# Performance work log

Hardware: AMD Instinct MI355X
Metric: run time of the kernel (lower is better)

The kernel has to match this reference:

```python
import jax, jax.numpy as jnp
import numpy as np

D = 768      # d_model
S = 8192     # wordpiece positions
N = 8192     # character rows
T = 1024     # words (token ids 1..T)
F = 16       # max_form_len
L = 8        # max_tag_len
XV = 50257   # xtokenizer vocab
CV = 512     # char vocab
TV = 512     # tag vocab


def setup_inputs() -> dict:
    key = jax.random.key(0)
    ks = jax.random.split(key, 16)
    xtokens = jax.random.randint(ks[0], (1, S), 0, XV)
    # tokens[:,:,0]=word id 1..T (each word owns a contiguous run of chars),
    # tokens[:,:,1]=xtoken position in [0,S), tokens[:,:,2]=char id
    tok_ids = (jnp.arange(N) * T) // N + 1
    xtok_ids = jax.random.randint(ks[1], (N,), 0, S)
    char_ids = jax.random.randint(ks[2], (N,), 0, CV)
    tokens = jnp.stack([tok_ids, xtok_ids, char_ids], axis=-1)[None]
    target_form_chars = jax.random.randint(ks[3], (1, T * F), 0, CV)
    target_tags = jax.random.randint(ks[4], (1, T * L), 0, TV)
    special_symbols = jnp.arange(4, dtype=jnp.int32)
    sc = 1.0 / np.sqrt(D)
    return {
        "xtokens": xtokens,
        "tokens": tokens,
        "special_symbols": special_symbols,
        "max_form_len": F,
        "max_tag_len": L,
        "target_form_chars": target_form_chars,
        "target_tags": target_tags,
        "xemb": jax.random.normal(ks[5], (XV, D), jnp.float32) * sc,
        "W_enc": jax.random.normal(ks[6], (D, D), jnp.float32) * sc,
        "b_enc": jnp.zeros((D,), jnp.float32),
        "char_emb": jax.random.normal(ks[7], (CV, D), jnp.float32) * sc,
        "tag_emb": jax.random.normal(ks[8], (TV, D), jnp.float32) * sc,
        "W_s": jax.random.normal(ks[9], (D, D), jnp.float32) * sc,
        "W_c": jax.random.normal(ks[10], (D, D), jnp.float32) * sc,
        "form_pos": jax.random.normal(ks[11], (F, D), jnp.float32) * sc,
        "tag_pos": jax.random.normal(ks[12], (L, D), jnp.float32) * sc,
        "W_char": jax.random.normal(ks[13], (D, CV), jnp.float32) * sc,
        "W_tag": jax.random.normal(ks[14], (D, TV), jnp.float32) * sc,
    }


def reference(xtokens, tokens, special_symbols, max_form_len, max_tag_len,
              target_form_chars, target_tags,
              xemb, W_enc, b_enc, char_emb, tag_emb,
              W_s, W_c, form_pos, tag_pos, W_char, W_tag):
    n_tok = target_form_chars.shape[1] // max_form_len  # = T (static)
    # xmodel: contextual encoding of wordpieces -> token_ctx [1,S,D]
    token_ctx = jnp.tanh(xemb[xtokens] @ W_enc + b_enc)
    # Vectorized replacement of the while-loop: per-word segment mean over
    # the xtoken positions of that word's characters (boolean-mask gather).
    seg = tokens[0, :, 0] - 1                     # [N] word index 0..T-1
    gathered = token_ctx[0][tokens[0, :, 1]]      # [N,D] gather ctx per char
    ones = jnp.ones((gathered.shape[0],), gathered.dtype)
    cnt = jax.ops.segment_sum(ones, seg, num_segments=n_tok)        # [T]
    token_state = jax.ops.segment_sum(gathered, seg, num_segments=n_tok)
    token_state = token_state / cnt[:, None]      # [T,D] mean-pooled state
    # character-level summary of input_chars (col 2), same segment mean
    char_in = char_emb[tokens[0, :, 2]]           # [N,D]
    char_state = jax.ops.segment_sum(char_in, seg, num_segments=n_tok)
    char_state = char_state / cnt[:, None]
    state = jnp.tanh(token_state @ W_s + char_state @ W_c)          # [T,D]
    # tagger decoding with teacher forcing on the sliced target sequences
    tgt_c = char_emb[target_form_chars[0].reshape(n_tok, max_form_len)]
    h_c = jnp.tanh(state[:, None, :] + form_pos[None, :, :] + tgt_c)
    seg_scores = (h_c @ W_char).reshape(1, n_tok * max_form_len, W_char.shape[1])
    tgt_t = tag_emb[target_tags[0].reshape(n_tok, max_tag_len)]
    h_t = jnp.tanh(state[:, None, :] + tag_pos[None, :, :] + tgt_t)
    tag_scores = (h_t @ W_tag).reshape(1, n_tok * max_tag_len, W_tag.shape[1])
    return seg_scores, tag_scores
```

## Files before the change

### kernel.cpp

```cpp
#include <hip/hip_runtime.h>
#include <hip/hip_bf16.h>

#define DD 768
#define NN 8192
#define TT 1024
#define FF 16
#define LL 8
#define CVV 512
#define TVV 512

typedef __attribute__((ext_vector_type(8))) short bf16x8;
typedef __attribute__((ext_vector_type(4))) float f32x4;

__device__ inline unsigned short f2bf(float f) {
    union { float f; unsigned u; } v; v.f = f;
    unsigned r = v.u + 0x7fffu + ((v.u >> 16) & 1u);
    return (unsigned short)(r >> 16);
}

__device__ inline float fast_tanh(float x) {
    float e2 = __expf(2.0f * x);
    return (e2 - 1.0f) * __builtin_amdgcn_rcpf(e2 + 1.0f);
}

__device__ inline void async16(const void* g, void* l) {
    __builtin_amdgcn_global_load_lds(
        (const __attribute__((address_space(1))) unsigned int*)g,
        (__attribute__((address_space(3))) unsigned int*)l, 16, 0, 0);
}

#define GEMM_PROLOG(COLT)                                                    \
    __shared__ short As[128 * 32];                                           \
    __shared__ short Bs[128 * 32];                                           \
    const int bcol = (blockIdx.x % (COLT)) * 128;                            \
    const int brow = (blockIdx.x / (COLT)) * 128;                            \
    const int t = threadIdx.x, lane = t & 63, wid = t >> 6;                  \
    const int wr = (wid >> 1) * 64, wc = (wid & 1) * 64;                     \
    const int l15 = lane & 15, lk8 = (lane >> 4) * 8;                        \
    const int strow = t >> 2, skb = (t & 3) * 8;                             \
    short* al0 = &As[t * 8];                                                 \
    short* al1 = &As[2048 + t * 8];                                          \
    short* bl0 = &Bs[t * 8];                                                 \
    short* bl1 = &Bs[2048 + t * 8];                                          \
    f32x4 acc[4][4] = {};

#define MFMA_TILE_CORE()                                                     \
    {                                                                        \
        bf16x8 afr[4], bfr[4];                                               \
        _Pragma("unroll")                                                    \
        for (int m = 0; m < 4; ++m)                                          \
            afr[m] = *(const bf16x8*)&As[(wr + m * 16 + l15) * 32 + lk8];    \
        _Pragma("unroll")                                                    \
        for (int n = 0; n < 4; ++n)                                          \
            bfr[n] = *(const bf16x8*)&Bs[(wc + n * 16 + l15) * 32 + lk8];    \
        _Pragma("unroll")                                                    \
        for (int m = 0; m < 4; ++m)                                          \
            _Pragma("unroll")                                                \
            for (int n = 0; n < 4; ++n)                                      \
                acc[m][n] = __builtin_amdgcn_mfma_f32_16x16x32_bf16(         \
                    afr[m], bfr[n], acc[m][n], 0, 0, 0);                     \
    }

#define GEMM_KLOOP(KTOT, APTR, BPTR, K)                                      \
    {                                                                        \
        const short* ag0 = (APTR) + (size_t)(brow + strow) * (K) + skb;      \
        const short* ag1 = (APTR) + (size_t)(brow + strow + 64) * (K) + skb; \
        const short* bg0 = (BPTR) + (size_t)(bcol + strow) * (K) + skb;      \
        const short* bg1 = (BPTR) + (size_t)(bcol + strow + 64) * (K) + skb; \
        for (int k0 = 0; k0 < (KTOT); k0 += 32) {                            \
            __syncthreads();                                                 \
            async16(ag0 + k0, al0);                                          \
            async16(ag1 + k0, al1);                                          \
            async16(bg0 + k0, bl0);                                          \
            async16(bg1 + k0, bl1);                                          \
            __syncthreads();                                                 \
            MFMA_TILE_CORE();                                                \
        }                                                                    \
    }

template<int M, int N, int K, int EPI>
__global__ __launch_bounds__(256) void k_gemm(
    const short* __restrict__ A, const short* __restrict__ B,
    const float* __restrict__ bias, float* __restrict__ C)
{
    GEMM_PROLOG(N / 128);
    GEMM_KLOOP(K, A, B, K);
    #pragma unroll
    for (int m = 0; m < 4; ++m)
        #pragma unroll
        for (int n = 0; n < 4; ++n) {
            int col = bcol + wc + n * 16 + l15;
            int row = brow + wr + m * 16 + (lane >> 4) * 4;
            float bv = (EPI == 1) ? bias[col] : 0.0f;
            #pragma unroll
            for (int r = 0; r < 4; ++r) {
                float v = acc[m][n][r] + bv;
                if (EPI == 1) v = fast_tanh(v);
                C[(size_t)(row + r) * N + col] = v;
            }
        }
}

__global__ __launch_bounds__(256) void k_state_gemm(
    const short* __restrict__ tS, const short* __restrict__ cS,
    const short* __restrict__ WsT, const short* __restrict__ WcT,
    float* __restrict__ state)
{
    GEMM_PROLOG(DD / 128);
    GEMM_KLOOP(DD, tS, WsT, DD);
    GEMM_KLOOP(DD, cS, WcT, DD);
    #pragma unroll
    for (int m = 0; m < 4; ++m)
        #pragma unroll
        for (int n = 0; n < 4; ++n) {
            int col = bcol + wc + n * 16 + l15;
            int row = brow + wr + m * 16 + (lane >> 4) * 4;
            #pragma unroll
            for (int r = 0; r < 4; ++r)
                state[(size_t)(row + r) * DD + col] = fast_tanh(acc[m][n][r]);
        }
}

__global__ __launch_bounds__(256) void k_transpose_all(
    const float* __restrict__ We, const float* __restrict__ Ws,
    const float* __restrict__ Wc, const float* __restrict__ Wch,
    const float* __restrict__ Wtg,
    short* eT, short* sT, short* cT, short* chT, short* tgT)
{
    __shared__ float ls[32][33];
    int b = blockIdx.x;
    const float* in; short* out; int C;
    if      (b < 576)  { in = We;  out = eT;  C = 768; }
    else if (b < 1152) { in = Ws;  out = sT;  C = 768; b -= 576; }
    else if (b < 1728) { in = Wc;  out = cT;  C = 768; b -= 1152; }
    else if (b < 2112) { in = Wch; out = chT; C = 512; b -= 1728; }
    else               { in = Wtg; out = tgT; C = 512; b -= 2112; }
    const int R = 768;
    int ct = C / 32;
    int bx = b % ct, by = b / ct;
    int t = threadIdx.x;
    int c = t & 31, r0 = (t >> 5) * 4;
    #pragma unroll
    for (int i = 0; i < 4; ++i)
        ls[r0 + i][c] = in[(size_t)(by * 32 + r0 + i) * C + bx * 32 + c];
    __syncthreads();
    int cc = t >> 3, rb = (t & 7) * 4;
    ushort4 v;
    v.x = f2bf(ls[rb + 0][cc]);
    v.y = f2bf(ls[rb + 1][cc]);
    v.z = f2bf(ls[rb + 2][cc]);
    v.w = f2bf(ls[rb + 3][cc]);
    *(ushort4*)&out[(size_t)(bx * 32 + cc) * R + by * 32 + rb] = v;
}

__global__ __launch_bounds__(256) void k_prep_ctx(
    const float* __restrict__ xemb, const int* __restrict__ xtokens,
    short* __restrict__ A)
{
    int e = (blockIdx.x * 256 + threadIdx.x) * 8;
    int i = e / DD, k = e % DD;
    const float* src = xemb + (size_t)xtokens[i] * DD + k;
    float4 v0 = ((const float4*)src)[0];
    float4 v1 = ((const float4*)src)[1];
    bf16x8 p;
    p[0] = f2bf(v0.x); p[1] = f2bf(v0.y); p[2] = f2bf(v0.z); p[3] = f2bf(v0.w);
    p[4] = f2bf(v1.x); p[5] = f2bf(v1.y); p[6] = f2bf(v1.z); p[7] = f2bf(v1.w);
    *(bf16x8*)(A + e) = p;
}

template<int PF>
__global__ __launch_bounds__(256) void k_prep_score(
    const float* __restrict__ state, const float* __restrict__ pos,
    const float* __restrict__ emb, const int* __restrict__ tgt,
    short* __restrict__ A)
{
    int e = (blockIdx.x * 256 + threadIdx.x) * 8;
    int i = e / DD, k = e % DD;
    const float* sp = state + (size_t)(i / PF) * DD + k;
    const float* pp = pos + (size_t)(i % PF) * DD + k;
    const float* ep = emb + (size_t)tgt[i] * DD + k;
    bf16x8 q;
    #pragma unroll
    for (int h = 0; h < 2; ++h) {
        float4 s = ((const float4*)sp)[h];
        float4 p = ((const float4*)pp)[h];
        float4 ev = ((const float4*)ep)[h];
        q[h * 4 + 0] = f2bf(fast_tanh(s.x + p.x + ev.x));
        q[h * 4 + 1] = f2bf(fast_tanh(s.y + p.y + ev.y));
        q[h * 4 + 2] = f2bf(fast_tanh(s.z + p.z + ev.z));
        q[h * 4 + 3] = f2bf(fast_tanh(s.w + p.w + ev.w));
    }
    *(bf16x8*)(A + e) = q;
}

__global__ __launch_bounds__(256) void k_segsum(
    const int* __restrict__ tokens, const float* __restrict__ token_ctx,
    const float* __restrict__ char_emb,
    short* __restrict__ tS, short* __restrict__ cS)
{
    int j = blockIdx.x;
    int lo = 0, hi = NN;
    while (lo < hi) { int mid = (lo + hi) >> 1; if (tokens[mid * 3] < j + 1) lo = mid + 1; else hi = mid; }
    int start = lo;
    hi = NN;
    while (lo < hi) { int mid = (lo + hi) >> 1; if (tokens[mid * 3] < j + 2) lo = mid + 1; else hi = mid; }
    int end = lo;

    float accT[3] = {0.f, 0.f, 0.f}, accC[3] = {0.f, 0.f, 0.f};
    for (int i = start; i < end; ++i) {
        int xid = tokens[i * 3 + 1];
        int cid = tokens[i * 3 + 2];
        const float* tr = token_ctx + (size_t)xid * DD;
        const float* cr = char_emb + (size_t)cid * DD;
        #pragma unroll
        for (int q = 0; q < 3; ++q) {
            int d = threadIdx.x + q * 256;
            accT[q] += tr[d];
            accC[q] += cr[d];
        }
    }
    float inv = 1.0f / (float)(end - start);
    #pragma unroll
    for (int q = 0; q < 3; ++q) {
        int d = threadIdx.x + q * 256;
        tS[(size_t)j * DD + d] = (short)f2bf(accT[q] * inv);
        cS[(size_t)j * DD + d] = (short)f2bf(accC[q] * inv);
    }
}

extern "C" void kernel_launch(void* const* d_in, const int* in_sizes, int n_in,
                              void* d_out, int out_size, void* d_ws, size_t ws_size,
                              hipStream_t stream)
{
    const int*   xtokens  = (const int*)d_in[0];
    const int*   tokens   = (const int*)d_in[1];
    const int*   tfc      = (const int*)d_in[5];
    const int*   ttg      = (const int*)d_in[6];
    const float* xemb     = (const float*)d_in[7];
    const float* W_enc    = (const float*)d_in[8];
    const float* b_enc    = (const float*)d_in[9];
    const float* char_emb = (const float*)d_in[10];
    const float* tag_emb  = (const float*)d_in[11];
    const float* W_s      = (const float*)d_in[12];
    const float* W_c      = (const float*)d_in[13];
    const float* form_pos = (const float*)d_in[14];
    const float* tag_pos  = (const float*)d_in[15];
    const float* W_char   = (const float*)d_in[16];
    const float* W_tag    = (const float*)d_in[17];
    float* out = (float*)d_out;
    float* ws  = (float*)d_ws;

    float* token_ctx = ws;
    float* state     = ws +  6291456;
    short* tS_bf     = (short*)(ws +  7077888);
    short* cS_bf     = (short*)(ws +  7471104);
    short* W_encT    = (short*)(ws +  7864320);
    short* W_sT      = (short*)(ws +  8159232);
    short* W_cT      = (short*)(ws +  8454144);
    short* W_charT   = (short*)(ws +  8749056);
    short* W_tagT    = (short*)(ws +  8945664);
    short* A_ctx     = (short*)(ws +  9142272);
    short* A_f       = (short*)(ws + 12288000);
    short* A_t       = (short*)(ws + 18579456);

    hipLaunchKernelGGL(k_transpose_all, dim3(2496), dim3(256), 0, stream,
                       W_enc, W_s, W_c, W_char, W_tag,
                       W_encT, W_sT, W_cT, W_charT, W_tagT);
    hipLaunchKernelGGL(k_prep_ctx, dim3(NN * DD / 2048), dim3(256), 0, stream,
                       xemb, xtokens, A_ctx);
    hipLaunchKernelGGL((k_gemm<NN, DD, DD, 1>), dim3((NN/128)*(DD/128)), dim3(256), 0, stream,
                       A_ctx, W_encT, b_enc, token_ctx);
    hipLaunchKernelGGL(k_segsum, dim3(TT), dim3(256), 0, stream,
                       tokens, token_ctx, char_emb, tS_bf, cS_bf);
    hipLaunchKernelGGL(k_state_gemm, dim3((TT/128)*(DD/128)), dim3(256), 0, stream,
                       tS_bf, cS_bf, W_sT, W_cT, state);
    hipLaunchKernelGGL((k_prep_score<FF>), dim3(TT * FF * DD / 2048), dim3(256), 0, stream,
                       state, form_pos, char_emb, tfc, A_f);
    hipLaunchKernelGGL((k_gemm<TT * FF, CVV, DD, 0>), dim3((TT*FF/128)*(CVV/128)), dim3(256), 0, stream,
                       A_f, W_charT, nullptr, out);
    hipLaunchKernelGGL((k_prep_score<LL>), dim3(TT * LL * DD / 2048), dim3(256), 0, stream,
                       state, tag_pos, tag_emb, ttg, A_t);
    hipLaunchKernelGGL((k_gemm<TT * LL, TVV, DD, 0>), dim3((TT*LL/128)*(TVV/128)), dim3(256), 0, stream,
                       A_t, W_tagT, nullptr, out + (size_t)TT * FF * CVV);
}
```

Baseline: 365.8 us.

## Double-buffer GEMM LDS tiles and merge prep/score launches into fewer kernels

The GEMM k-loop now uses two LDS buffers, so the async global-to-LDS load of the next K slice is issued before the MFMAs on the current slice, with one barrier per iteration instead of two. The transpose and context-prep kernels are fused into one launch. The form and tag prep and score GEMMs are each merged into a single launch, picking the weight matrix per row block and writing contiguous output. This cuts launch count and tail effects, and hides load latency behind compute, at the cost of twice the LDS per block and possible occupancy changes.

```diff
diff --git a/kernel.cpp b/kernel.cpp
--- a/kernel.cpp
+++ b/kernel.cpp
@@ -30,29 +30,31 @@
 }
 
 #define GEMM_PROLOG(COLT)                                                    \
-    __shared__ short As[128 * 32];                                           \
-    __shared__ short Bs[128 * 32];                                           \
+    __shared__ short As[2][128 * 32];                                        \
+    __shared__ short Bs[2][128 * 32];                                        \
     const int bcol = (blockIdx.x % (COLT)) * 128;                            \
     const int brow = (blockIdx.x / (COLT)) * 128;                            \
     const int t = threadIdx.x, lane = t & 63, wid = t >> 6;                  \
     const int wr = (wid >> 1) * 64, wc = (wid & 1) * 64;                     \
     const int l15 = lane & 15, lk8 = (lane >> 4) * 8;                        \
     const int strow = t >> 2, skb = (t & 3) * 8;                             \
-    short* al0 = &As[t * 8];                                                 \
-    short* al1 = &As[2048 + t * 8];                                          \
-    short* bl0 = &Bs[t * 8];                                                 \
-    short* bl1 = &Bs[2048 + t * 8];                                          \
     f32x4 acc[4][4] = {};
 
-#define MFMA_TILE_CORE()                                                     \
+#define STAGE_AB(c, k0)                                                      \
+    async16(ag0 + (k0), &As[c][t * 8]);                                      \
+    async16(ag1 + (k0), &As[c][2048 + t * 8]);                               \
+    async16(bg0 + (k0), &Bs[c][t * 8]);                                      \
+    async16(bg1 + (k0), &Bs[c][2048 + t * 8]);
+
+#define MFMA_TILE_CORE(c)                                                    \
     {                                                                        \
         bf16x8 afr[4], bfr[4];                                               \
         _Pragma("unroll")                                                    \
         for (int m = 0; m < 4; ++m)                                          \
-            afr[m] = *(const bf16x8*)&As[(wr + m * 16 + l15) * 32 + lk8];    \
+            afr[m] = *(const bf16x8*)&As[c][(wr + m * 16 + l15) * 32 + lk8]; \
         _Pragma("unroll")                                                    \
         for (int n = 0; n < 4; ++n)                                          \
-            bfr[n] = *(const bf16x8*)&Bs[(wc + n * 16 + l15) * 32 + lk8];    \
+            bfr[n] = *(const bf16x8*)&Bs[c][(wc + n * 16 + l15) * 32 + lk8]; \
         _Pragma("unroll")                                                    \
         for (int m = 0; m < 4; ++m)                                          \
             _Pragma("unroll")                                                \
@@ -67,38 +69,40 @@
         const short* ag1 = (APTR) + (size_t)(brow + strow + 64) * (K) + skb; \
         const short* bg0 = (BPTR) + (size_t)(bcol + strow) * (K) + skb;      \
         const short* bg1 = (BPTR) + (size_t)(bcol + strow + 64) * (K) + skb; \
+        STAGE_AB(0, 0);                                                      \
+        __syncthreads();                                                     \
+        int cur = 0;                                                         \
         for (int k0 = 0; k0 < (KTOT); k0 += 32) {                            \
+            if (k0 + 32 < (KTOT)) { STAGE_AB(cur ^ 1, k0 + 32); }            \
+            MFMA_TILE_CORE(cur);                                             \
             __syncthreads();                                                 \
-            async16(ag0 + k0, al0);                                          \
-            async16(ag1 + k0, al1);                                          \
-            async16(bg0 + k0, bl0);                                          \
-            async16(bg1 + k0, bl1);                                          \
-            __syncthreads();                                                 \
-            MFMA_TILE_CORE();                                                \
+            cur ^= 1;                                                        \
         }                                                                    \
     }
 
-template<int M, int N, int K, int EPI>
-__global__ __launch_bounds__(256) void k_gemm(
+#define GEMM_EPILOG(NV, DST, DO_TANH, BIASP)                                 \
+    _Pragma("unroll")                                                        \
+    for (int m = 0; m < 4; ++m)                                              \
+        _Pragma("unroll")                                                    \
+        for (int n = 0; n < 4; ++n) {                                        \
+            int col = bcol + wc + n * 16 + l15;                              \
+            int row = brow + wr + m * 16 + (lane >> 4) * 4;                  \
+            float bv = (DO_TANH && (BIASP)) ? ((const float*)(BIASP))[col] : 0.0f; \
+            _Pragma("unroll")                                                \
+            for (int r = 0; r < 4; ++r) {                                    \
+                float v = acc[m][n][r] + bv;                                 \
+                if (DO_TANH) v = fast_tanh(v);                               \
+                (DST)[(size_t)(row + r) * (NV) + col] = v;                   \
+            }                                                                \
+        }
+
+__global__ __launch_bounds__(256) void k_gemm_ctx(
     const short* __restrict__ A, const short* __restrict__ B,
     const float* __restrict__ bias, float* __restrict__ C)
 {
-    GEMM_PROLOG(N / 128);
-    GEMM_KLOOP(K, A, B, K);
-    #pragma unroll
-    for (int m = 0; m < 4; ++m)
-        #pragma unroll
-        for (int n = 0; n < 4; ++n) {
-            int col = bcol + wc + n * 16 + l15;
-            int row = brow + wr + m * 16 + (lane >> 4) * 4;
-            float bv = (EPI == 1) ? bias[col] : 0.0f;
-            #pragma unroll
-            for (int r = 0; r < 4; ++r) {
-                float v = acc[m][n][r] + bv;
-                if (EPI == 1) v = fast_tanh(v);
-                C[(size_t)(row + r) * N + col] = v;
-            }
-        }
+    GEMM_PROLOG(DD / 128);
+    GEMM_KLOOP(DD, A, B, DD);
+    GEMM_EPILOG(DD, C, 1, bias);
 }
 
 __global__ __launch_bounds__(256) void k_state_gemm(
@@ -109,76 +113,85 @@
     GEMM_PROLOG(DD / 128);
     GEMM_KLOOP(DD, tS, WsT, DD);
     GEMM_KLOOP(DD, cS, WcT, DD);
-    #pragma unroll
-    for (int m = 0; m < 4; ++m)
-        #pragma unroll
-        for (int n = 0; n < 4; ++n) {
-            int col = bcol + wc + n * 16 + l15;
-            int row = brow + wr + m * 16 + (lane >> 4) * 4;
-            #pragma unroll
-            for (int r = 0; r < 4; ++r)
-                state[(size_t)(row + r) * DD + col] = fast_tanh(acc[m][n][r]);
-        }
-}
-
-__global__ __launch_bounds__(256) void k_transpose_all(
+    GEMM_EPILOG(DD, state, 1, (const float*)nullptr);
+}
+
+__global__ __launch_bounds__(256) void k_gemm_scores(
+    const short* __restrict__ A, const short* __restrict__ Bch,
+    const short* __restrict__ Btg, float* __restrict__ C)
+{
+    GEMM_PROLOG(CVV / 128);
+    const short* B = (brow >= TT * FF) ? Btg : Bch;
+    GEMM_KLOOP(DD, A, B, DD);
+    GEMM_EPILOG(CVV, C, 0, (const float*)nullptr);
+}
+
+__global__ __launch_bounds__(256) void k_front(
     const float* __restrict__ We, const float* __restrict__ Ws,
     const float* __restrict__ Wc, const float* __restrict__ Wch,
     const float* __restrict__ Wtg,
-    short* eT, short* sT, short* cT, short* chT, short* tgT)
+    short* eT, short* sT, short* cT, short* chT, short* tgT,
+    const float* __restrict__ xemb, const int* __restrict__ xtokens,
+    short* __restrict__ A)
 {
     __shared__ float ls[32][33];
     int b = blockIdx.x;
-    const float* in; short* out; int C;
-    if      (b < 576)  { in = We;  out = eT;  C = 768; }
-    else if (b < 1152) { in = Ws;  out = sT;  C = 768; b -= 576; }
-    else if (b < 1728) { in = Wc;  out = cT;  C = 768; b -= 1152; }
-    else if (b < 2112) { in = Wch; out = chT; C = 512; b -= 1728; }
-    else               { in = Wtg; out = tgT; C = 512; b -= 2112; }
-    const int R = 768;
-    int ct = C / 32;
-    int bx = b % ct, by = b / ct;
     int t = threadIdx.x;
-    int c = t & 31, r0 = (t >> 5) * 4;
-    #pragma unroll
-    for (int i = 0; i < 4; ++i)
-        ls[r0 + i][c] = in[(size_t)(by * 32 + r0 + i) * C + bx * 32 + c];
-    __syncthreads();
-    int cc = t >> 3, rb = (t & 7) * 4;
-    ushort4 v;
-    v.x = f2bf(ls[rb + 0][cc]);
-    v.y = f2bf(ls[rb + 1][cc]);
-    v.z = f2bf(ls[rb + 2][cc]);
-    v.w = f2bf(ls[rb + 3][cc]);
-    *(ushort4*)&out[(size_t)(bx * 32 + cc) * R + by * 32 + rb] = v;
-}
-
-__global__ __launch_bounds__(256) void k_prep_ctx(
-    const float* __restrict__ xemb, const int* __restrict__ xtokens,
+    if (b < 2496) {
+        const float* in; short* out; int C;
+        if      (b < 576)  { in = We;  out = eT;  C = 768; }
+        else if (b < 1152) { in = Ws;  out = sT;  C = 768; b -= 576; }
+        else if (b < 1728) { in = Wc;  out = cT;  C = 768; b -= 1152; }
+        else if (b < 2112) { in = Wch; out = chT; C = 512; b -= 1728; }
+        else               { in = Wtg; out = tgT; C = 512; b -= 2112; }
+        const int R = 768;
+        int ct = C / 32;
+        int bx = b % ct, by = b / ct;
+        int c = t & 31, r0 = (t >> 5) * 4;
+        #pragma unroll
+        for (int i = 0; i < 4; ++i)
+            ls[r0 + i][c] = in[(size_t)(by * 32 + r0 + i) * C + bx * 32 + c];
+        __syncthreads();
+        int cc = t >> 3, rb = (t & 7) * 4;
+        ushort4 v;
+        v.x = f2bf(ls[rb + 0][cc]);
+        v.y = f2bf(ls[rb + 1][cc]);
+        v.z = f2bf(ls[rb + 2][cc]);
+        v.w = f2bf(ls[rb + 3][cc]);
+        *(ushort4*)&out[(size_t)(bx * 32 + cc) * R + by * 32 + rb] = v;
+    } else {
+        int e = ((b - 2496) * 256 + t) * 8;
+        int i = e / DD, k = e % DD;
+        const float* src = xemb + (size_t)xtokens[i] * DD + k;
+        float4 v0 = ((const float4*)src)[0];
+        float4 v1 = ((const float4*)src)[1];
+        bf16x8 p;
+        p[0] = f2bf(v0.x); p[1] = f2bf(v0.y); p[2] = f2bf(v0.z); p[3] = f2bf(v0.w);
+        p[4] = f2bf(v1.x); p[5] = f2bf(v1.y); p[6] = f2bf(v1.z); p[7] = f2bf(v1.w);
+        *(bf16x8*)(A + e) = p;
+    }
+}
+
+__global__ __launch_bounds__(256) void k_prep_scores(
+    const float* __restrict__ state,
+    const float* __restrict__ form_pos, const float* __restrict__ tag_pos,
+    const float* __restrict__ char_emb, const float* __restrict__ tag_emb,
+    const int* __restrict__ tfc, const int* __restrict__ ttg,
     short* __restrict__ A)
 {
     int e = (blockIdx.x * 256 + threadIdx.x) * 8;
     int i = e / DD, k = e % DD;
-    const float* src = xemb + (size_t)xtokens[i] * DD + k;
-    float4 v0 = ((const float4*)src)[0];
-    float4 v1 = ((const float4*)src)[1];
-    bf16x8 p;
-    p[0] = f2bf(v0.x); p[1] = f2bf(v0.y); p[2] = f2bf(v0.z); p[3] = f2bf(v0.w);
-    p[4] = f2bf(v1.x); p[5] = f2bf(v1.y); p[6] = f2bf(v1.z); p[7] = f2bf(v1.w);
-    *(bf16x8*)(A + e) = p;
-}
-
-template<int PF>
-__global__ __launch_bounds__(256) void k_prep_score(
-    const float* __restrict__ state, const float* __restrict__ pos,
-    const float* __restrict__ emb, const int* __restrict__ tgt,
-    short* __restrict__ A)
-{
-    int e = (blockIdx.x * 256 + threadIdx.x) * 8;
-    int i = e / DD, k = e % DD;
-    const float* sp = state + (size_t)(i / PF) * DD + k;
-    const float* pp = pos + (size_t)(i % PF) * DD + k;
-    const float* ep = emb + (size_t)tgt[i] * DD + k;
+    const float *sp, *pp, *ep;
+    if (i < TT * FF) {
+        sp = state + (size_t)(i / FF) * DD + k;
+        pp = form_pos + (size_t)(i % FF) * DD + k;
+        ep = char_emb + (size_t)tfc[i] * DD + k;
+    } else {
+        int j = i - TT * FF;
+        sp = state + (size_t)(j / LL) * DD + k;
+        pp = tag_pos + (size_t)(j % LL) * DD + k;
+        ep = tag_emb + (size_t)ttg[j] * DD + k;
+    }
     bf16x8 q;
     #pragma unroll
     for (int h = 0; h < 2; ++h) {
@@ -260,26 +273,20 @@
     short* W_charT   = (short*)(ws +  8749056);
     short* W_tagT    = (short*)(ws +  8945664);
     short* A_ctx     = (short*)(ws +  9142272);
-    short* A_f       = (short*)(ws + 12288000);
-    short* A_t       = (short*)(ws + 18579456);
-
-    hipLaunchKernelGGL(k_transpose_all, dim3(2496), dim3(256), 0, stream,
+    short* A_sc      = (short*)(ws + 12288000);
+
+    hipLaunchKernelGGL(k_front, dim3(5568), dim3(256), 0, stream,
                        W_enc, W_s, W_c, W_char, W_tag,
-                       W_encT, W_sT, W_cT, W_charT, W_tagT);
-    hipLaunchKernelGGL(k_prep_ctx, dim3(NN * DD / 2048), dim3(256), 0, stream,
+                       W_encT, W_sT, W_cT, W_charT, W_tagT,
                        xemb, xtokens, A_ctx);
-    hipLaunchKernelGGL((k_gemm<NN, DD, DD, 1>), dim3((NN/128)*(DD/128)), dim3(256), 0, stream,
+    hipLaunchKernelGGL(k_gemm_ctx, dim3((NN/128)*(DD/128)), dim3(256), 0, stream,
                        A_ctx, W_encT, b_enc, token_ctx);
     hipLaunchKernelGGL(k_segsum, dim3(TT), dim3(256), 0, stream,
                        tokens, token_ctx, char_emb, tS_bf, cS_bf);
     hipLaunchKernelGGL(k_state_gemm, dim3((TT/128)*(DD/128)), dim3(256), 0, stream,
                        tS_bf, cS_bf, W_sT, W_cT, state);
-    hipLaunchKernelGGL((k_prep_score<FF>), dim3(TT * FF * DD / 2048), dim3(256), 0, stream,
-                       state, form_pos, char_emb, tfc, A_f);
-    hipLaunchKernelGGL((k_gemm<TT * FF, CVV, DD, 0>), dim3((TT*FF/128)*(CVV/128)), dim3(256), 0, stream,
-                       A_f, W_charT, nullptr, out);
-    hipLaunchKernelGGL((k_prep_score<LL>), dim3(TT * LL * DD / 2048), dim3(256), 0, stream,
-                       state, tag_pos, tag_emb, ttg, A_t);
-    hipLaunchKernelGGL((k_gemm<TT * LL, TVV, DD, 0>), dim3((TT*LL/128)*(TVV/128)), dim3(256), 0, stream,
-                       A_t, W_tagT, nullptr, out + (size_t)TT * FF * CVV);
-}
+    hipLaunchKernelGGL(k_prep_scores, dim3((TT*(FF+LL)) * DD / 2048), dim3(256), 0, stream,
+                       state, form_pos, tag_pos, char_emb, tag_emb, tfc, ttg, A_sc);
+    hipLaunchKernelGGL(k_gemm_scores, dim3((TT*(FF+LL)/128)*(CVV/128)), dim3(256), 0, stream,
+                       A_sc, W_charT, W_tagT, out);
+}
```

Measured after the change: 348.9 us. -4.6%, faster.
